# Kernel optimization log

Hardware: AMD Instinct MI355X
Metric: run time of the kernel (lower is better)

Reference implementation:

```python
import jax, jax.numpy as jnp
import numpy as np

HEADS = 4
DIM_HEAD = 32
SCALE = 10.0
EPS = 1e-12  # F.normalize eps


def setup_inputs() -> dict:
    key = jax.random.key(0)
    k0, k1, k2 = jax.random.split(key, 3)
    b, c, h, w = 4, 256, 64, 64
    hidden = HEADS * DIM_HEAD  # 128
    x = jax.random.normal(k0, (b, c, h, w), dtype=jnp.float32)
    # 1x1 convs == per-pixel linear layers; store as [out_ch, in_ch]
    w_qkv = jax.random.normal(k1, (3 * hidden, c), dtype=jnp.float32) * (1.0 / np.sqrt(c))
    w_out = jax.random.normal(k2, (c, hidden), dtype=jnp.float32) * (1.0 / np.sqrt(hidden))
    b_out = jnp.zeros((c,), dtype=jnp.float32)
    return {"x": x, "w_qkv": w_qkv, "w_out": w_out, "b_out": b_out}


def _l2norm(t):
    # normalize along the per-head feature dim d (axis=2 of [b,h,d,n])
    n = jnp.sqrt(jnp.sum(t * t, axis=2, keepdims=True))
    return t / jnp.maximum(n, EPS)


def reference(x, w_qkv, w_out, b_out):
    b, c, h, w = x.shape
    n = h * w
    # to_qkv 1x1 conv (no bias)
    qkv = jnp.einsum('oc,bchw->bohw', w_qkv, x)          # [b, 3*hidden, h, w]
    qkv = qkv.reshape(b, 3, HEADS, DIM_HEAD, n)          # chunk dim=1 then split heads
    q, k, v = qkv[:, 0], qkv[:, 1], qkv[:, 2]            # each [b, heads, d, n]
    q = _l2norm(q)
    k = _l2norm(k)
    sim = jnp.einsum('bhdi,bhdj->bhij', q, k) * SCALE    # [b, heads, n, n]
    attn = jax.nn.softmax(sim, axis=-1)
    out = jnp.einsum('bhij,bhdj->bhid', attn, v)         # [b, heads, n, d]
    # 'b h (x y) d -> b (h d) x y'
    out = out.transpose(0, 1, 3, 2).reshape(b, HEADS * DIM_HEAD, h, w)
    # to_out 1x1 conv with bias
    return jnp.einsum('oc,bchw->bohw', w_out, out) + b_out[None, :, None, None]
```

## Files before the change

### kernel.cpp

```cpp
#include <hip/hip_runtime.h>
#include <math.h>

#define BB 4
#define CC 256
#define NHEAD 4
#define DH 32
#define NN 4096
#define HID 128

typedef _Float16 f16;
typedef _Float16 f16x8 __attribute__((ext_vector_type(8)));
typedef _Float16 f16x4 __attribute__((ext_vector_type(4)));
typedef float f32x4 __attribute__((ext_vector_type(4)));
typedef unsigned int u32x4 __attribute__((ext_vector_type(4)));

#define QPRESCALE 14.42695041f
#define NSHIFT 14.42695041f

#if __has_builtin(__builtin_amdgcn_exp2f)
#define EXP2F(x) __builtin_amdgcn_exp2f(x)
#else
#define EXP2F(x) __expf((x)*0.6931471805599453f)
#endif

__device__ __forceinline__ f16x8 cvt8(const float* p) {
    float4 a = *(const float4*)p;
    float4 b = *(const float4*)(p + 4);
    f16x8 r;
    r[0] = (f16)a.x; r[1] = (f16)a.y; r[2] = (f16)a.z; r[3] = (f16)a.w;
    r[4] = (f16)b.x; r[5] = (f16)b.y; r[6] = (f16)b.z; r[7] = (f16)b.w;
    return r;
}

__global__ __launch_bounds__(256) void qkv_fused(const float* __restrict__ x,
                                                 const float* __restrict__ wq,
                                                 f16* __restrict__ qh,
                                                 f16* __restrict__ kh,
                                                 f16* __restrict__ vh) {
    int wave = threadIdx.x >> 6, lane = threadIdx.x & 63;
    int quad = lane >> 4, col = lane & 15;
    int b = blockIdx.z;
    int o0 = blockIdx.y * 64;
    int i0 = blockIdx.x * 128 + wave * 32;
    const float* xb = x + (size_t)b * CC * NN;

    f32x4 c[4][2];
#pragma unroll
    for (int mt = 0; mt < 4; mt++)
#pragma unroll
        for (int nt = 0; nt < 2; nt++) c[mt][nt] = f32x4{0.f, 0.f, 0.f, 0.f};

#pragma unroll
    for (int k0 = 0; k0 < CC; k0 += 32) {
        f16x8 a[4];
#pragma unroll
        for (int mt = 0; mt < 4; mt++)
            a[mt] = cvt8(wq + (size_t)(o0 + mt * 16 + col) * CC + k0 + quad * 8);
#pragma unroll
        for (int nt = 0; nt < 2; nt++) {
            const float* xc = xb + (size_t)(k0 + quad * 8) * NN + i0 + nt * 16 + col;
            f16x8 bf;
#pragma unroll
            for (int j = 0; j < 8; j++) bf[j] = (f16)xc[(size_t)j * NN];
#pragma unroll
            for (int mt = 0; mt < 4; mt++)
                c[mt][nt] = __builtin_amdgcn_mfma_f32_16x16x32_f16(a[mt], bf, c[mt][nt], 0, 0, 0);
        }
    }

    if (o0 < 256) {
        int isQ = (o0 < 128);
        int obase = isQ ? o0 : (o0 - 128);
        f16* dst = isQ ? qh : kh;
        float pre = isQ ? QPRESCALE : 1.0f;
#pragma unroll
        for (int nt = 0; nt < 2; nt++) {
#pragma unroll
            for (int hh = 0; hh < 2; hh++) {
                float ss = 0.f;
#pragma unroll
                for (int m2 = 0; m2 < 2; m2++)
#pragma unroll
                    for (int r = 0; r < 4; r++) {
                        float v = c[hh * 2 + m2][nt][r];
                        ss = fmaf(v, v, ss);
                    }
                ss += __shfl_xor(ss, 16);
                ss += __shfl_xor(ss, 32);
                float inv = pre / fmaxf(sqrtf(ss), 1e-12f);
                int h = (obase + hh * 32) >> 5;
                size_t row = ((size_t)(b * 4 + h) * NN + i0 + nt * 16 + col) * 32;
#pragma unroll
                for (int m2 = 0; m2 < 2; m2++) {
                    f16x4 st;
#pragma unroll
                    for (int r = 0; r < 4; r++) st[r] = (f16)(c[hh * 2 + m2][nt][r] * inv);
                    *(f16x4*)(dst + row + m2 * 16 + quad * 4) = st;
                }
            }
        }
    } else {
        int o2 = o0 - 256;
#pragma unroll
        for (int nt = 0; nt < 2; nt++) {
            int i = i0 + nt * 16 + col;
#pragma unroll
            for (int mt = 0; mt < 4; mt++) {
                int h = (o2 + mt * 16) >> 5;
                int d = (mt & 1) * 16 + quad * 4;
#pragma unroll
                for (int r = 0; r < 4; r++)
                    vh[((size_t)(b * 4 + h) * 32 + d + r) * NN + i] = (f16)c[mt][nt][r];
            }
        }
    }
}

#define KROW 40
#define VROW 72

__device__ __forceinline__ f16x8 expblk2(f32x4 sa, f32x4 sb) {
    u32x4 w;
    w[0] = __builtin_bit_cast(unsigned int,
            __builtin_amdgcn_cvt_pkrtz(EXP2F(sa[0]), EXP2F(sa[1])));
    w[1] = __builtin_bit_cast(unsigned int,
            __builtin_amdgcn_cvt_pkrtz(EXP2F(sa[2]), EXP2F(sa[3])));
    w[2] = __builtin_bit_cast(unsigned int,
            __builtin_amdgcn_cvt_pkrtz(EXP2F(sb[0]), EXP2F(sb[1])));
    w[3] = __builtin_bit_cast(unsigned int,
            __builtin_amdgcn_cvt_pkrtz(EXP2F(sb[2]), EXP2F(sb[3])));
    return __builtin_bit_cast(f16x8, w);
}

__device__ __forceinline__ void compute_g(const f16* kl, const f16* vl, int jb,
                                          int col, int quad, const f16x8 (&qB)[4],
                                          f32x4 (&o)[4][2], f32x4 (&lf)[4]) {
    f16x8 kA = *(const f16x8*)(kl + (jb + col) * KROW + quad * 8);
    f16x8 kB = *(const f16x8*)(kl + (jb + 16 + col) * KROW + quad * 8);
    f16x8 v0 = *(const f16x8*)(vl + col * VROW + jb + quad * 8);
    f16x8 v1 = *(const f16x8*)(vl + (16 + col) * VROW + jb + quad * 8);
    const f32x4 zs = {-NSHIFT, -NSHIFT, -NSHIFT, -NSHIFT};
    f16 one = (f16)1.0f;
    f16x8 ones = {one, one, one, one, one, one, one, one};
#pragma unroll
    for (int f = 0; f < 4; f++) {
        f32x4 sa = __builtin_amdgcn_mfma_f32_16x16x32_f16(kA, qB[f], zs, 0, 0, 0);
        f32x4 sb = __builtin_amdgcn_mfma_f32_16x16x32_f16(kB, qB[f], zs, 0, 0, 0);
        f16x8 p = expblk2(sa, sb);
        o[f][0] = __builtin_amdgcn_mfma_f32_16x16x32_f16(p, v0, o[f][0], 0, 0, 0);
        o[f][1] = __builtin_amdgcn_mfma_f32_16x16x32_f16(p, v1, o[f][1], 0, 0, 0);
        lf[f]   = __builtin_amdgcn_mfma_f32_16x16x32_f16(p, ones, lf[f], 0, 0, 0);
    }
}

template <int SPLIT>
__global__ __launch_bounds__(256, 4) void attn_mfma(const f16* __restrict__ qh,
                                                    const f16* __restrict__ kh,
                                                    const f16* __restrict__ vh,
                                                    float* __restrict__ op,
                                                    float* __restrict__ lp,
                                                    f16* __restrict__ att16) {
    __shared__ __align__(16) f16 klds[2][64 * KROW];
    __shared__ __align__(16) f16 vlds[2][32 * VROW];
    int t = threadIdx.x;
    int wave = t >> 6, lane = t & 63;
    int quad = lane >> 4, col = lane & 15;

    int bid = blockIdx.x;
    int xcd = bid & 7;
    int slot = bid >> 3;
    int bh = xcd * 2 + slot / (16 * SPLIT);
    int rem = slot % (16 * SPLIT);
    int s = rem >> 4;
    int i0 = (rem & 15) * 256;
    int iw = i0 + wave * 64;

    const int NT = 64 / SPLIT;
    int kbase = s * (NN / SPLIT);

    const f16* qb = qh + (size_t)bh * NN * 32;
    const f16* kb = kh + (size_t)bh * NN * 32 + (size_t)kbase * 32;
    const f16* vb = vh + (size_t)bh * 32 * NN + kbase;

    f16x8 qB[4];
#pragma unroll
    for (int f = 0; f < 4; f++)
        qB[f] = *(const f16x8*)(qb + (size_t)(iw + f * 16 + col) * 32 + quad * 8);

    f32x4 o[4][2], lf[4];
#pragma unroll
    for (int f = 0; f < 4; f++) {
        o[f][0] = f32x4{0.f, 0.f, 0.f, 0.f};
        o[f][1] = f32x4{0.f, 0.f, 0.f, 0.f};
        lf[f]   = f32x4{0.f, 0.f, 0.f, 0.f};
    }

    int ktr = t >> 2, kts = t & 3;
    int ksrc = (ktr & 32) | ((ktr & 12) << 1) | ((ktr & 16) >> 2) | (ktr & 3);
    int vtr = t >> 3, vts = t & 7;

    f16x8 kr, vr;
    kr = *(const f16x8*)(kb + (size_t)(0 + ksrc) * 32 + kts * 8);
    vr = *(const f16x8*)(vb + (size_t)vtr * NN + 0 + vts * 8);
    *(f16x8*)(&klds[0][0] + ktr * KROW + kts * 8) = kr;
    *(f16x8*)(&vlds[0][0] + vtr * VROW + vts * 8) = vr;
    __syncthreads();
    kr = *(const f16x8*)(kb + (size_t)(64 + ksrc) * 32 + kts * 8);
    vr = *(const f16x8*)(vb + (size_t)vtr * NN + 64 + vts * 8);

    for (int tile = 0; tile < NT - 2; tile++) {
        int buf = tile & 1;
        const f16* kl = &klds[buf][0];
        const f16* vl = &vlds[buf][0];
        compute_g(kl, vl, 0, col, quad, qB, o, lf);
        compute_g(kl, vl, 32, col, quad, qB, o, lf);
        *(f16x8*)(&klds[buf ^ 1][0] + ktr * KROW + kts * 8) = kr;
        *(f16x8*)(&vlds[buf ^ 1][0] + vtr * VROW + vts * 8) = vr;
        __syncthreads();
        int j0 = (tile + 2) * 64;
        kr = *(const f16x8*)(kb + (size_t)(j0 + ksrc) * 32 + kts * 8);
        vr = *(const f16x8*)(vb + (size_t)vtr * NN + j0 + vts * 8);
    }
    {
        compute_g(&klds[0][0], &vlds[0][0], 0, col, quad, qB, o, lf);
        compute_g(&klds[0][0], &vlds[0][0], 32, col, quad, qB, o, lf);
        *(f16x8*)(&klds[1][0] + ktr * KROW + kts * 8) = kr;
        *(f16x8*)(&vlds[1][0] + vtr * VROW + vts * 8) = vr;
        __syncthreads();
    }
    {
        compute_g(&klds[1][0], &vlds[1][0], 0, col, quad, qB, o, lf);
        compute_g(&klds[1][0], &vlds[1][0], 32, col, quad, qB, o, lf);
    }

    if constexpr (SPLIT == 1) {
        int b = bh >> 2, h = bh & 3;
        f16* ab = att16 + (size_t)b * NN * HID + h * 32;
#pragma unroll
        for (int f = 0; f < 4; f++)
#pragma unroll
            for (int r = 0; r < 4; r++) {
                float inv = __builtin_amdgcn_rcpf(lf[f][r]);
                size_t row = (size_t)(iw + f * 16 + quad * 4 + r) * HID;
                ab[row + col]      = (f16)(o[f][0][r] * inv);
                ab[row + 16 + col] = (f16)(o[f][1][r] * inv);
            }
    } else {
        float* ob = op + (size_t)(s * 16 + bh) * NN * 32;
#pragma unroll
        for (int f = 0; f < 4; f++)
#pragma unroll
            for (int r = 0; r < 4; r++) {
                size_t rr = (size_t)(iw + f * 16 + quad * 4 + r) * 32;
                ob[rr + col]      = o[f][0][r];
                ob[rr + 16 + col] = o[f][1][r];
            }
        if (col == 0) {
            float* lb = lp + (size_t)(s * 16 + bh) * NN;
#pragma unroll
            for (int f = 0; f < 4; f++)
#pragma unroll
                for (int r = 0; r < 4; r++)
                    lb[iw + f * 16 + quad * 4 + r] = lf[f][r];
        }
    }
}

__global__ __launch_bounds__(256) void attn_combine(const float* __restrict__ op,
                                                    const float* __restrict__ lp,
                                                    f16* __restrict__ att16,
                                                    int nsplit) {
    int gid = blockIdx.x * 256 + threadIdx.x;
    int rowid = gid >> 3;
    int seg = gid & 7;
    int bh = rowid >> 12;
    int q = rowid & 4095;

    float l = 0.f;
    f32x4 acc = {0.f, 0.f, 0.f, 0.f};
    for (int s = 0; s < nsplit; s++) {
        l += lp[(size_t)(s * 16 + bh) * NN + q];
        f32x4 a = *(const f32x4*)(op + ((size_t)(s * 16 + bh) * NN + q) * 32 + seg * 4);
        acc += a;
    }
    float inv = __builtin_amdgcn_rcpf(l);
    int b = bh >> 2, h = bh & 3;
    f16x4 st;
    st[0] = (f16)(acc[0] * inv);
    st[1] = (f16)(acc[1] * inv);
    st[2] = (f16)(acc[2] * inv);
    st[3] = (f16)(acc[3] * inv);
    *(f16x4*)(att16 + ((size_t)b * NN + q) * HID + h * 32 + seg * 4) = st;
}

__global__ __launch_bounds__(256) void out_mfma(const f16* __restrict__ att16,
                                                const float* __restrict__ wo,
                                                const float* __restrict__ bo,
                                                float* __restrict__ out) {
    int wave = threadIdx.x >> 6, lane = threadIdx.x & 63;
    int quad = lane >> 4, col = lane & 15;
    int b = blockIdx.z;
    int i0 = (blockIdx.x * 4 + wave) * 32;
    int o0 = blockIdx.y * 64;
    const f16* ab = att16 + (size_t)b * NN * HID;

    const f32x4 z = {0.f, 0.f, 0.f, 0.f};
    f32x4 c[2][4];
#pragma unroll
    for (int it = 0; it < 2; it++)
#pragma unroll
        for (int ot = 0; ot < 4; ot++) c[it][ot] = z;

#pragma unroll
    for (int k0 = 0; k0 < HID; k0 += 32) {
        f16x8 a0 = *(const f16x8*)(ab + (size_t)(i0 + col) * HID + k0 + quad * 8);
        f16x8 a1 = *(const f16x8*)(ab + (size_t)(i0 + 16 + col) * HID + k0 + quad * 8);
#pragma unroll
        for (int ot = 0; ot < 4; ot++) {
            f16x8 bf = cvt8(wo + (size_t)(o0 + ot * 16 + col) * HID + k0 + quad * 8);
            c[0][ot] = __builtin_amdgcn_mfma_f32_16x16x32_f16(a0, bf, c[0][ot], 0, 0, 0);
            c[1][ot] = __builtin_amdgcn_mfma_f32_16x16x32_f16(a1, bf, c[1][ot], 0, 0, 0);
        }
    }

#pragma unroll
    for (int it = 0; it < 2; it++)
#pragma unroll
        for (int ot = 0; ot < 4; ot++) {
            int o = o0 + ot * 16 + col;
            float bias = bo[o];
            int i = i0 + it * 16 + quad * 4;
            float4 st = {c[it][ot][0] + bias, c[it][ot][1] + bias,
                         c[it][ot][2] + bias, c[it][ot][3] + bias};
            *(float4*)(out + ((size_t)b * CC + o) * NN + i) = st;
        }
}

extern "C" void kernel_launch(void* const* d_in, const int* in_sizes, int n_in,
                              void* d_out, int out_size, void* d_ws, size_t ws_size,
                              hipStream_t stream) {
    const float* x     = (const float*)d_in[0];
    const float* w_qkv = (const float*)d_in[1];
    const float* w_out = (const float*)d_in[2];
    const float* b_out = (const float*)d_in[3];
    float* out = (float*)d_out;

    char* ws = (char*)d_ws;
    f16* qh    = (f16*)(ws);
    f16* kh    = (f16*)(ws + (4u << 20));
    f16* vh    = (f16*)(ws + (8u << 20));
    f16* att16 = (f16*)(ws + (12u << 20));

    qkv_fused<<<dim3(NN / 128, 384 / 64, BB), 256, 0, stream>>>(x, w_qkv, qh, kh, vh);

    if (ws_size >= (50ull << 20)) {
        float* op = (float*)(ws + (16ull << 20));
        float* lp = (float*)(ws + (48ull << 20));
        attn_mfma<4><<<dim3(1024), 256, 0, stream>>>(qh, kh, vh, op, lp, att16);
        attn_combine<<<dim3(2048), 256, 0, stream>>>(op, lp, att16, 4);
    } else if (ws_size >= (33ull << 20)) {
        float* op = (float*)(ws + (16ull << 20));
        float* lp = (float*)(ws + (32ull << 20));
        attn_mfma<2><<<dim3(512), 256, 0, stream>>>(qh, kh, vh, op, lp, att16);
        attn_combine<<<dim3(2048), 256, 0, stream>>>(op, lp, att16, 2);
    } else {
        attn_mfma<1><<<dim3(256), 256, 0, stream>>>(qh, kh, vh, nullptr, nullptr, att16);
    }

    out_mfma<<<dim3(NN / 128, CC / 64, BB), 256, 0, stream>>>(att16, w_out, b_out, out);
}
```

Before: 155.0 us.

## Pre-transpose input and weights to fp16 before QKV projection GEMM

Adds a prep kernel that transposes x into a channel-contiguous fp16 layout and converts the QKV and output weights to fp16. A new qkv16 kernel then runs the projection on contiguous f16x8 loads instead of converting fp32 on the fly, and out_mfma reads pre-converted fp16 weights. The aim is to remove the strided fp32 loads and repeated conversions inside the GEMM loops. In exchange it adds an extra launch and an extra round trip of x through memory, and it reuses the op buffer region as xt scratch.

```diff
diff --git a/kernel.cpp b/kernel.cpp
--- a/kernel.cpp
+++ b/kernel.cpp
@@ -11,6 +11,7 @@
 typedef _Float16 f16;
 typedef _Float16 f16x8 __attribute__((ext_vector_type(8)));
 typedef _Float16 f16x4 __attribute__((ext_vector_type(4)));
+typedef _Float16 f16x2 __attribute__((ext_vector_type(2)));
 typedef float f32x4 __attribute__((ext_vector_type(4)));
 typedef unsigned int u32x4 __attribute__((ext_vector_type(4)));
 
@@ -30,6 +31,139 @@
     r[0] = (f16)a.x; r[1] = (f16)a.y; r[2] = (f16)a.z; r[3] = (f16)a.w;
     r[4] = (f16)b.x; r[5] = (f16)b.y; r[6] = (f16)b.z; r[7] = (f16)b.w;
     return r;
+}
+
+__global__ __launch_bounds__(256) void prep(const float* __restrict__ x,
+                                            const float* __restrict__ wq,
+                                            const float* __restrict__ wo,
+                                            f16* __restrict__ xt,
+                                            f16* __restrict__ w16,
+                                            f16* __restrict__ wo16) {
+    int tb = blockIdx.x;
+    if (tb < 512) {
+        __shared__ f16 tile[256][36];
+        int b = tb >> 7, rem = tb & 127;
+        int c0 = (rem >> 4) << 5;
+        int i0 = (rem & 15) << 8;
+        const float* xb = x + ((size_t)b * CC + c0) * NN + i0;
+        int rp = threadIdx.x >> 4;
+        int seg = threadIdx.x & 15;
+#pragma unroll
+        for (int pass = 0; pass < 4; pass++) {
+            int i = pass * 64 + seg * 4;
+            float4 a = *(const float4*)(xb + (size_t)(2 * rp) * NN + i);
+            float4 bq = *(const float4*)(xb + (size_t)(2 * rp + 1) * NN + i);
+#pragma unroll
+            for (int j = 0; j < 4; j++) {
+                f16x2 pr;
+                float aj = (j == 0) ? a.x : (j == 1) ? a.y : (j == 2) ? a.z : a.w;
+                float bj = (j == 0) ? bq.x : (j == 1) ? bq.y : (j == 2) ? bq.z : bq.w;
+                pr[0] = (f16)aj;
+                pr[1] = (f16)bj;
+                *(f16x2*)(&tile[i + j][2 * rp]) = pr;
+            }
+        }
+        __syncthreads();
+        f16* dst = xt + ((size_t)b * NN + i0) * CC + c0;
+        int cq = threadIdx.x & 7;
+        int ii = threadIdx.x >> 3;
+#pragma unroll
+        for (int pass = 0; pass < 8; pass++) {
+            int i = pass * 32 + ii;
+            *(f16x4*)(dst + (size_t)i * CC + cq * 4) = *(const f16x4*)(&tile[i][cq * 4]);
+        }
+    } else {
+        int k = tb - 512;
+        const float* src = (k < 3) ? (wq + (size_t)k * 32768) : wo;
+        f16* dst = (k < 3) ? (w16 + (size_t)k * 32768) : wo16;
+        for (int e = threadIdx.x; e < 8192; e += 256) {
+            float4 a = ((const float4*)src)[e];
+            f16x4 s;
+            s[0] = (f16)a.x; s[1] = (f16)a.y; s[2] = (f16)a.z; s[3] = (f16)a.w;
+            ((f16x4*)dst)[e] = s;
+        }
+    }
+}
+
+__global__ __launch_bounds__(256) void qkv16(const f16* __restrict__ xt,
+                                             const f16* __restrict__ w16,
+                                             f16* __restrict__ qh,
+                                             f16* __restrict__ kh,
+                                             f16* __restrict__ vh) {
+    int wave = threadIdx.x >> 6, lane = threadIdx.x & 63;
+    int quad = lane >> 4, col = lane & 15;
+    int b = blockIdx.z;
+    int o0 = blockIdx.y * 64;
+    int i0 = blockIdx.x * 128 + wave * 32;
+    const f16* xb = xt + (size_t)b * NN * CC;
+
+    f32x4 c[4][2];
+#pragma unroll
+    for (int mt = 0; mt < 4; mt++)
+#pragma unroll
+        for (int nt = 0; nt < 2; nt++) c[mt][nt] = f32x4{0.f, 0.f, 0.f, 0.f};
+
+#pragma unroll
+    for (int k0 = 0; k0 < CC; k0 += 32) {
+        f16x8 a[4];
+#pragma unroll
+        for (int mt = 0; mt < 4; mt++)
+            a[mt] = *(const f16x8*)(w16 + (size_t)(o0 + mt * 16 + col) * CC + k0 + quad * 8);
+#pragma unroll
+        for (int nt = 0; nt < 2; nt++) {
+            f16x8 bf = *(const f16x8*)(xb + (size_t)(i0 + nt * 16 + col) * CC + k0 + quad * 8);
+#pragma unroll
+            for (int mt = 0; mt < 4; mt++)
+                c[mt][nt] = __builtin_amdgcn_mfma_f32_16x16x32_f16(a[mt], bf, c[mt][nt], 0, 0, 0);
+        }
+    }
+
+    if (o0 < 256) {
+        int isQ = (o0 < 128);
+        int obase = isQ ? o0 : (o0 - 128);
+        f16* dst = isQ ? qh : kh;
+        float pre = isQ ? QPRESCALE : 1.0f;
+#pragma unroll
+        for (int nt = 0; nt < 2; nt++) {
+#pragma unroll
+            for (int hh = 0; hh < 2; hh++) {
+                float ss = 0.f;
+#pragma unroll
+                for (int m2 = 0; m2 < 2; m2++)
+#pragma unroll
+                    for (int r = 0; r < 4; r++) {
+                        float v = c[hh * 2 + m2][nt][r];
+                        ss = fmaf(v, v, ss);
+                    }
+                ss += __shfl_xor(ss, 16);
+                ss += __shfl_xor(ss, 32);
+                float inv = pre / fmaxf(sqrtf(ss), 1e-12f);
+                int h = (obase + hh * 32) >> 5;
+                size_t row = ((size_t)(b * 4 + h) * NN + i0 + nt * 16 + col) * 32;
+#pragma unroll
+                for (int m2 = 0; m2 < 2; m2++) {
+                    f16x4 st;
+#pragma unroll
+                    for (int r = 0; r < 4; r++) st[r] = (f16)(c[hh * 2 + m2][nt][r] * inv);
+                    *(f16x4*)(dst + row + m2 * 16 + quad * 4) = st;
+                }
+            }
+        }
+    } else {
+        int o2 = o0 - 256;
+#pragma unroll
+        for (int nt = 0; nt < 2; nt++) {
+            int i = i0 + nt * 16 + col;
+#pragma unroll
+            for (int mt = 0; mt < 4; mt++) {
+                int h = (o2 + mt * 16) >> 5;
+                int d = (mt & 1) * 16 + quad * 4;
+#pragma unroll
+                for (int r = 0; r < 4; r++)
+                    vh[((size_t)(b * 4 + h) * 32 + d + r) * NN + i] = (f16)c[mt][nt][r];
+            }
+        }
+    }
 }
 
 __global__ __launch_bounds__(256) void qkv_fused(const float* __restrict__ x,
@@ -293,8 +427,10 @@
     *(f16x4*)(att16 + ((size_t)b * NN + q) * HID + h * 32 + seg * 4) = st;
 }
 
+template <bool W16>
 __global__ __launch_bounds__(256) void out_mfma(const f16* __restrict__ att16,
                                                 const float* __restrict__ wo,
+                                                const f16* __restrict__ wo16,
                                                 const float* __restrict__ bo,
                                                 float* __restrict__ out) {
     int wave = threadIdx.x >> 6, lane = threadIdx.x & 63;
@@ -317,7 +453,11 @@
         f16x8 a1 = *(const f16x8*)(ab + (size_t)(i0 + 16 + col) * HID + k0 + quad * 8);
 #pragma unroll
         for (int ot = 0; ot < 4; ot++) {
-            f16x8 bf = cvt8(wo + (size_t)(o0 + ot * 16 + col) * HID + k0 + quad * 8);
+            f16x8 bf;
+            if constexpr (W16)
+                bf = *(const f16x8*)(wo16 + (size_t)(o0 + ot * 16 + col) * HID + k0 + quad * 8);
+            else
+                bf = cvt8(wo + (size_t)(o0 + ot * 16 + col) * HID + k0 + quad * 8);
             c[0][ot] = __builtin_amdgcn_mfma_f32_16x16x32_f16(a0, bf, c[0][ot], 0, 0, 0);
             c[1][ot] = __builtin_amdgcn_mfma_f32_16x16x32_f16(a1, bf, c[1][ot], 0, 0, 0);
         }
@@ -350,22 +490,31 @@
     f16* kh    = (f16*)(ws + (4u << 20));
     f16* vh    = (f16*)(ws + (8u << 20));
     f16* att16 = (f16*)(ws + (12u << 20));
-
-    qkv_fused<<<dim3(NN / 128, 384 / 64, BB), 256, 0, stream>>>(x, w_qkv, qh, kh, vh);
+    f16* xt = (f16*)(ws + (16ull << 20));
 
     if (ws_size >= (50ull << 20)) {
         float* op = (float*)(ws + (16ull << 20));
         float* lp = (float*)(ws + (48ull << 20));
+        f16* wo16 = (f16*)(ws + (49ull << 20));
+        f16* w16  = (f16*)(ws + (49ull << 20) + (64u << 10));
+        prep<<<dim3(516), 256, 0, stream>>>(x, w_qkv, w_out, xt, w16, wo16);
+        qkv16<<<dim3(NN / 128, 384 / 64, BB), 256, 0, stream>>>(xt, w16, qh, kh, vh);
         attn_mfma<4><<<dim3(1024), 256, 0, stream>>>(qh, kh, vh, op, lp, att16);
         attn_combine<<<dim3(2048), 256, 0, stream>>>(op, lp, att16, 4);
+        out_mfma<true><<<dim3(NN / 128, CC / 64, BB), 256, 0, stream>>>(att16, w_out, wo16, b_out, out);
     } else if (ws_size >= (33ull << 20)) {
         float* op = (float*)(ws + (16ull << 20));
         float* lp = (float*)(ws + (32ull << 20));
+        f16* wo16 = (f16*)(ws + (32ull << 20) + (512u << 10));
+        f16* w16  = (f16*)(ws + (32ull << 20) + (576u << 10));
+        prep<<<dim3(516), 256, 0, stream>>>(x, w_qkv, w_out, xt, w16, wo16);
+        qkv16<<<dim3(NN / 128, 384 / 64, BB), 256, 0, stream>>>(xt, w16, qh, kh, vh);
         attn_mfma<2><<<dim3(512), 256, 0, stream>>>(qh, kh, vh, op, lp, att16);
         attn_combine<<<dim3(2048), 256, 0, stream>>>(op, lp, att16, 2);
+        out_mfma<true><<<dim3(NN / 128, CC / 64, BB), 256, 0, stream>>>(att16, w_out, wo16, b_out, out);
     } else {
+        qkv_fused<<<dim3(NN / 128, 384 / 64, BB), 256, 0, stream>>>(x, w_qkv, qh, kh, vh);
         attn_mfma<1><<<dim3(256), 256, 0, stream>>>(qh, kh, vh, nullptr, nullptr, att16);
-    }
-
-    out_mfma<<<dim3(NN / 128, CC / 64, BB), 256, 0, stream>>>(att16, w_out, b_out, out);
-}
+        out_mfma<false><<<dim3(NN / 128, CC / 64, BB), 256, 0, stream>>>(att16, w_out, nullptr, b_out, out);
+    }
+}
```

Result: slower. 158.4 us (+2.2%).

## Compute all QKV outputs per block with coalesced LDS-staged input tile

Applied to the files above, without the earlier changes.

The QKV projection kernel now makes each block compute all 384 output channels for a 32-pixel tile. Each wave covers 96 channels, and the x tile is staged through shared memory with coalesced float4 loads and converted to fp16 once. Before, the grid was split across six output-channel groups, so x was re-read from global memory once per group, using strided scalar loads. The change removes that redundant x traffic but adds two barriers per k-step, and each wave now holds more accumulator registers.

```diff
diff --git a/kernel.cpp b/kernel.cpp
--- a/kernel.cpp
+++ b/kernel.cpp
@@ -32,51 +32,60 @@
     return r;
 }
 
-__global__ __launch_bounds__(256) void qkv_fused(const float* __restrict__ x,
-                                                 const float* __restrict__ wq,
-                                                 f16* __restrict__ qh,
-                                                 f16* __restrict__ kh,
-                                                 f16* __restrict__ vh) {
-    int wave = threadIdx.x >> 6, lane = threadIdx.x & 63;
+#define XROW 40
+
+__global__ __launch_bounds__(256) void qkv_mega(const float* __restrict__ x,
+                                                const float* __restrict__ wq,
+                                                f16* __restrict__ qh,
+                                                f16* __restrict__ kh,
+                                                f16* __restrict__ vh) {
+    __shared__ __align__(16) f16 xl[32 * XROW];
+    int t = threadIdx.x;
+    int wave = t >> 6, lane = t & 63;
     int quad = lane >> 4, col = lane & 15;
     int b = blockIdx.z;
-    int o0 = blockIdx.y * 64;
-    int i0 = blockIdx.x * 128 + wave * 32;
-    const float* xb = x + (size_t)b * CC * NN;
-
-    f32x4 c[4][2];
-#pragma unroll
-    for (int mt = 0; mt < 4; mt++)
+    int i0 = blockIdx.x * 32;
+    int o0w = wave * 96;
+
+    int sc = t >> 3;
+    int iseg = t & 7;
+    const float* xb = x + (size_t)b * CC * NN + i0 + iseg * 4;
+
+    f32x4 c[6][2];
+#pragma unroll
+    for (int mt = 0; mt < 6; mt++)
 #pragma unroll
         for (int nt = 0; nt < 2; nt++) c[mt][nt] = f32x4{0.f, 0.f, 0.f, 0.f};
 
 #pragma unroll
     for (int k0 = 0; k0 < CC; k0 += 32) {
-        f16x8 a[4];
-#pragma unroll
-        for (int mt = 0; mt < 4; mt++)
-            a[mt] = cvt8(wq + (size_t)(o0 + mt * 16 + col) * CC + k0 + quad * 8);
-#pragma unroll
-        for (int nt = 0; nt < 2; nt++) {
-            const float* xc = xb + (size_t)(k0 + quad * 8) * NN + i0 + nt * 16 + col;
-            f16x8 bf;
-#pragma unroll
-            for (int j = 0; j < 8; j++) bf[j] = (f16)xc[(size_t)j * NN];
-#pragma unroll
-            for (int mt = 0; mt < 4; mt++)
-                c[mt][nt] = __builtin_amdgcn_mfma_f32_16x16x32_f16(a[mt], bf, c[mt][nt], 0, 0, 0);
-        }
-    }
-
-    if (o0 < 256) {
-        int isQ = (o0 < 128);
-        int obase = isQ ? o0 : (o0 - 128);
-        f16* dst = isQ ? qh : kh;
-        float pre = isQ ? QPRESCALE : 1.0f;
-#pragma unroll
-        for (int nt = 0; nt < 2; nt++) {
-#pragma unroll
-            for (int hh = 0; hh < 2; hh++) {
+        float4 xv = *(const float4*)(xb + (size_t)(k0 + sc) * NN);
+        __syncthreads();
+        xl[(iseg * 4 + 0) * XROW + sc] = (f16)xv.x;
+        xl[(iseg * 4 + 1) * XROW + sc] = (f16)xv.y;
+        xl[(iseg * 4 + 2) * XROW + sc] = (f16)xv.z;
+        xl[(iseg * 4 + 3) * XROW + sc] = (f16)xv.w;
+        __syncthreads();
+        f16x8 bf0 = *(const f16x8*)(xl + (size_t)col * XROW + quad * 8);
+        f16x8 bf1 = *(const f16x8*)(xl + (size_t)(16 + col) * XROW + quad * 8);
+#pragma unroll
+        for (int mt = 0; mt < 6; mt++) {
+            f16x8 a = cvt8(wq + (size_t)(o0w + mt * 16 + col) * CC + k0 + quad * 8);
+            c[mt][0] = __builtin_amdgcn_mfma_f32_16x16x32_f16(a, bf0, c[mt][0], 0, 0, 0);
+            c[mt][1] = __builtin_amdgcn_mfma_f32_16x16x32_f16(a, bf1, c[mt][1], 0, 0, 0);
+        }
+    }
+
+#pragma unroll
+    for (int hh = 0; hh < 3; hh++) {
+        int oh = o0w + hh * 32;
+        if (oh < 256) {
+            int isQ = (oh < 128);
+            f16* dst = isQ ? qh : kh;
+            int h = (isQ ? oh : (oh - 128)) >> 5;
+            float pre = isQ ? QPRESCALE : 1.0f;
+#pragma unroll
+            for (int nt = 0; nt < 2; nt++) {
                 float ss = 0.f;
 #pragma unroll
                 for (int m2 = 0; m2 < 2; m2++)
@@ -88,7 +97,6 @@
                 ss += __shfl_xor(ss, 16);
                 ss += __shfl_xor(ss, 32);
                 float inv = pre / fmaxf(sqrtf(ss), 1e-12f);
-                int h = (obase + hh * 32) >> 5;
                 size_t row = ((size_t)(b * 4 + h) * NN + i0 + nt * 16 + col) * 32;
 #pragma unroll
                 for (int m2 = 0; m2 < 2; m2++) {
@@ -98,19 +106,17 @@
                     *(f16x4*)(dst + row + m2 * 16 + quad * 4) = st;
                 }
             }
-        }
-    } else {
-        int o2 = o0 - 256;
-#pragma unroll
-        for (int nt = 0; nt < 2; nt++) {
-            int i = i0 + nt * 16 + col;
-#pragma unroll
-            for (int mt = 0; mt < 4; mt++) {
-                int h = (o2 + mt * 16) >> 5;
-                int d = (mt & 1) * 16 + quad * 4;
-#pragma unroll
-                for (int r = 0; r < 4; r++)
-                    vh[((size_t)(b * 4 + h) * 32 + d + r) * NN + i] = (f16)c[mt][nt][r];
+        } else {
+            int h = (oh - 256) >> 5;
+#pragma unroll
+            for (int nt = 0; nt < 2; nt++) {
+                int i = i0 + nt * 16 + col;
+#pragma unroll
+                for (int m2 = 0; m2 < 2; m2++)
+#pragma unroll
+                    for (int r = 0; r < 4; r++)
+                        vh[((size_t)(b * 4 + h) * 32 + m2 * 16 + quad * 4 + r) * NN + i] =
+                            (f16)c[hh * 2 + m2][nt][r];
             }
         }
     }
@@ -351,7 +357,7 @@
     f16* vh    = (f16*)(ws + (8u << 20));
     f16* att16 = (f16*)(ws + (12u << 20));
 
-    qkv_fused<<<dim3(NN / 128, 384 / 64, BB), 256, 0, stream>>>(x, w_qkv, qh, kh, vh);
+    qkv_mega<<<dim3(NN / 32, 1, BB), 256, 0, stream>>>(x, w_qkv, qh, kh, vh);
 
     if (ws_size >= (50ull << 20)) {
         float* op = (float*)(ws + (16ull << 20));
```

After: 153.5 us. About the same (-1.0%).
